# Kernel optimization log

Measured on AMD Instinct MI355X. Metric: run time of the kernel, lower is better.

Reference implementation:

```python
import jax, jax.numpy as jnp
import numpy as np

# ---- config (matches init_kwargs) ----
DIM = 1024
HEADS = 8            # local_heads == heads
QK_HD = 128          # qk_head_dim
V_HD = 128           # v_head_dim
NOPE = 64            # qk_nope_head_dim
ROPE = 64            # qk_rope_head_dim
KV_LORA = 256
N_EXP = 32
N_GROUPS = 8
TOPK = 4             # n_activated_experts
TOPK_GROUPS = 4
INTER = 512
N_SHARED = 1
ROUTE_SCALE = 1.0
EPS = 1e-6


def rmsnorm(x, w):
    xf = x.astype(jnp.float32)
    rms = jnp.sqrt(jnp.mean(xf ** 2, axis=-1, keepdims=True) + EPS)
    return (xf / rms * w).astype(x.dtype)


def setup_inputs() -> dict:
    key = jax.random.key(0)
    ks = jax.random.split(key, 16)
    s = 0.02
    return {
        "x": jax.random.normal(ks[0], (2, 1024, DIM), jnp.float32),
        # attention sub-layer params
        "norm_attn": jnp.ones((DIM,), jnp.float32),
        "wq": jax.random.normal(ks[1], (DIM, HEADS * QK_HD), jnp.float32) * s,
        "wkv_a": jax.random.normal(ks[2], (DIM, KV_LORA + ROPE), jnp.float32) * s,
        "kv_norm_w": jnp.ones((KV_LORA,), jnp.float32),
        "wkv_b": jax.random.normal(ks[3], (KV_LORA, HEADS * (NOPE + V_HD)), jnp.float32) * s,
        "wo": jax.random.normal(ks[4], (HEADS * V_HD, DIM), jnp.float32) * s,
        # MoE sub-layer params
        "norm_moe": jnp.ones((DIM,), jnp.float32),
        "gate_w": jax.random.normal(ks[5], (N_EXP, DIM), jnp.float32) * 0.01,
        "gate_b": jnp.zeros((N_EXP,), jnp.float32),
        "ew1": jax.random.normal(ks[6], (N_EXP, DIM, INTER), jnp.float32) * s,
        "ew2": jax.random.normal(ks[7], (N_EXP, INTER, DIM), jnp.float32) * s,
        "ew3": jax.random.normal(ks[8], (N_EXP, DIM, INTER), jnp.float32) * s,
        "sw1": jax.random.normal(ks[9], (DIM, N_SHARED * INTER), jnp.float32) * s,
        "sw2": jax.random.normal(ks[10], (N_SHARED * INTER, DIM), jnp.float32) * s,
        "sw3": jax.random.normal(ks[11], (DIM, N_SHARED * INTER), jnp.float32) * s,
    }


def _mla(x, wq, wkv_a, kv_norm_w, wkv_b, wo):
    B, S, _ = x.shape
    # q_lora_rank == 0 -> direct q projection; nope/rope split+concat is identity
    q = (x @ wq).reshape(B, S, HEADS, QK_HD)
    kv = x @ wkv_a                                   # [B,S,KV_LORA+ROPE]
    c, k_pe = kv[..., :KV_LORA], kv[..., KV_LORA:]
    kvp = (rmsnorm(c, kv_norm_w) @ wkv_b).reshape(B, S, HEADS, NOPE + V_HD)
    k_nope, v = kvp[..., :NOPE], kvp[..., NOPE:]
    k = jnp.concatenate(
        [k_nope, jnp.broadcast_to(k_pe[:, :, None, :], (B, S, HEADS, ROPE))], axis=-1)
    out = jax.nn.dot_product_attention(q, k, v, scale=QK_HD ** -0.5, is_causal=True)
    return out.reshape(B, S, -1) @ wo


def _gate(xf, gate_w, gate_b):
    T = xf.shape[0]
    scores = jax.nn.sigmoid(xf @ gate_w.T)           # [T,E]
    original = scores
    s = scores + gate_b
    # hierarchical group selection: top-2 score sum per group, keep top groups
    sg = s.reshape(T, N_GROUPS, -1)
    group_score = jnp.sort(sg, axis=-1)[..., -2:].sum(axis=-1)
    group_idx = jnp.argsort(group_score, axis=-1)[..., -TOPK_GROUPS:]
    mask = jnp.ones((T, N_GROUPS), bool).at[jnp.arange(T)[:, None], group_idx].set(False)
    s = jnp.where(mask[..., None], -jnp.inf, sg).reshape(T, -1)
    indices = jnp.argsort(s, axis=-1)[..., -TOPK:]   # [T,K]
    w = jnp.take_along_axis(original, indices, axis=1)
    w = w / (w.sum(axis=-1, keepdims=True) + 1e-20)  # sigmoid normalization
    return w * ROUTE_SCALE, indices


def _moe(xf, gate_w, gate_b, ew1, ew2, ew3, sw1, sw2, sw3):
    # dense all-expert SwiGLU as in the original (nn.vmap over axis_size=E)
    weights, indices = _gate(xf, gate_w, gate_b)
    h = jax.nn.silu(jnp.einsum('td,edh->eth', xf, ew1)) * jnp.einsum('td,edh->eth', xf, ew3)
    all_out = jnp.einsum('eth,ehd->etd', h, ew2)     # [E,T,dim]
    # per-token gather of its top-k experts, weighted combine
    selected = jnp.take_along_axis(all_out.transpose(1, 0, 2), indices[:, :, None], axis=1)  # [T,K,dim]
    y = (selected * weights[..., None]).sum(axis=1)
    z = (jax.nn.silu(xf @ sw1) * (xf @ sw3)) @ sw2   # shared expert MLP
    return y + z


def reference(x, norm_attn, wq, wkv_a, kv_norm_w, wkv_b, wo,
              norm_moe, gate_w, gate_b, ew1, ew2, ew3, sw1, sw2, sw3):
    # MLA layer: x + MLA(RMSNorm(x))
    x = x + _mla(rmsnorm(x, norm_attn), wq, wkv_a, kv_norm_w, wkv_b, wo)
    # MoE layer: x + MoE(RMSNorm(x))
    shape = x.shape
    xf = rmsnorm(x, norm_moe).reshape(-1, DIM)
    y = _moe(xf, gate_w, gate_b, ew1, ew2, ew3, sw1, sw2, sw3)
    return x + y.reshape(shape)
```

## Files before the change

### kernel.cpp

```cpp
#include <hip/hip_runtime.h>
#include <hip/hip_bf16.h>

#define T_TOK 2048
#define DIM 1024
#define HEADS 8
#define QK_HD 128
#define V_HD 128
#define NOPE 64
#define ROPE 64
#define KV_LORA 256
#define N_EXP 32
#define TOPK 4
#define INTER 512
#define S_LEN 1024
#define KVP_W (HEADS * (NOPE + V_HD))

typedef __attribute__((ext_vector_type(8))) _Float16 f16x8;
typedef __attribute__((ext_vector_type(4))) float f32x4;

__device__ inline unsigned short f2h(float f) {
  union { _Float16 h; unsigned short u; } c;
  c.h = (_Float16)f;
  return c.u;
}
__device__ inline float h2f(unsigned short u) {
  union { _Float16 h; unsigned short u; } c;
  c.u = u;
  return (float)c.h;
}

__device__ inline int smask(int row) { return (row & 7) ^ ((row & 3) << 1); }
__device__ inline int swz(int row, int col) {
  return row * 64 + (col ^ (smask(row) << 3));
}

__device__ inline void gl16(const void* g, void* l) {
  __builtin_amdgcn_global_load_lds(
      (const __attribute__((address_space(1))) void*)g,
      (__attribute__((address_space(3))) void*)l, 16, 0, 0);
}

__launch_bounds__(256)
__global__ void tcvt_k(const float* __restrict__ src, unsigned short* __restrict__ dst,
                       int K, int N) {
  int e = blockIdx.z;
  src += (size_t)e * K * N;
  dst += (size_t)e * K * N;
  int n0 = blockIdx.x * 32, k0 = blockIdx.y * 32;
  __shared__ float ts[32][33];
  int tid = threadIdx.x;
  int r = tid >> 3, c4 = (tid & 7) * 4;
  float4 v = *(const float4*)(src + (size_t)(k0 + r) * N + n0 + c4);
  ts[r][c4] = v.x; ts[r][c4 + 1] = v.y; ts[r][c4 + 2] = v.z; ts[r][c4 + 3] = v.w;
  __syncthreads();
  ushort4 o;
  o.x = f2h(ts[c4][r]);
  o.y = f2h(ts[c4 + 1][r]);
  o.z = f2h(ts[c4 + 2][r]);
  o.w = f2h(ts[c4 + 3][r]);
  *(ushort4*)(dst + (size_t)(n0 + r) * K + k0 + c4) = o;
}

__launch_bounds__(64)
__global__ void zero_counters_k(int* __restrict__ counts, int* __restrict__ fill) {
  int i = threadIdx.x;
  if (i < N_EXP) { counts[i] = 0; fill[i] = 0; }
}

__launch_bounds__(256)
__global__ void rmsnorm_k(const float* __restrict__ x, int in_stride, int width,
                          const float* __restrict__ w, unsigned short* __restrict__ out,
                          float* __restrict__ out2, int out_stride) {
  int row = blockIdx.x;
  const float* xr = x + (size_t)row * in_stride;
  float ss = 0.f;
  for (int i = threadIdx.x; i < width; i += 256) { float v = xr[i]; ss += v * v; }
  #pragma unroll
  for (int off = 32; off; off >>= 1) ss += __shfl_down(ss, off, 64);
  __shared__ float red[4];
  if ((threadIdx.x & 63) == 0) red[threadIdx.x >> 6] = ss;
  __syncthreads();
  if (threadIdx.x == 0) {
    float tot = red[0] + red[1] + red[2] + red[3];
    red[0] = rsqrtf(tot / (float)width + 1e-6f);
  }
  __syncthreads();
  float scale = red[0];
  for (int i = threadIdx.x; i < width; i += 256) {
    float v = xr[i] * scale * w[i];
    out[(size_t)row * out_stride + i] = f2h(v);
    if (out2) out2[(size_t)row * out_stride + i] = v;
  }
}

template <int RES, int OUTH>
__launch_bounds__(256)
__global__ void gemm_bt_k(const unsigned short* __restrict__ A,
                          const unsigned short* __restrict__ B,
                          const float* __restrict__ R, void* __restrict__ Cout,
                          int N, int K) {
  const int n0 = blockIdx.x * 64;
  const int m0 = blockIdx.y * 64;
  __shared__ __align__(16) unsigned short As[64 * 64];
  __shared__ __align__(16) unsigned short Bs[64 * 64];
  const int tid = threadIdx.x;
  const int lane = tid & 63, wave = tid >> 6;
  const int quad = lane >> 4, lm = lane & 15;
  const int wm = (wave >> 1) * 32, wn = (wave & 1) * 32;
  f32x4 acc[2][2] = {};
  const int r0 = wave * 16 + (lane >> 3), r1 = r0 + 8;
  const int c0 = ((lane & 7) ^ smask(r0)) * 8;
  const int c1 = ((lane & 7) ^ smask(r1)) * 8;
  const unsigned short* A0 = A + (size_t)(m0 + r0) * K + c0;
  const unsigned short* A1 = A + (size_t)(m0 + r1) * K + c1;
  const unsigned short* B0 = B + (size_t)(n0 + r0) * K + c0;
  const unsigned short* B1 = B + (size_t)(n0 + r1) * K + c1;
  unsigned short* lA0 = &As[(size_t)(wave * 16) * 64];
  unsigned short* lA1 = &As[(size_t)(wave * 16 + 8) * 64];
  unsigned short* lB0 = &Bs[(size_t)(wave * 16) * 64];
  unsigned short* lB1 = &Bs[(size_t)(wave * 16 + 8) * 64];
  for (int k0 = 0; k0 < K; k0 += 64) {
    __syncthreads();
    gl16(A0 + k0, lA0);
    gl16(A1 + k0, lA1);
    gl16(B0 + k0, lB0);
    gl16(B1 + k0, lB1);
    __syncthreads();
    #pragma unroll
    for (int ks = 0; ks < 2; ks++) {
      f16x8 af0 = *(const f16x8*)&As[swz(wm + lm, ks * 32 + quad * 8)];
      f16x8 af1 = *(const f16x8*)&As[swz(wm + 16 + lm, ks * 32 + quad * 8)];
      f16x8 bf0 = *(const f16x8*)&Bs[swz(wn + lm, ks * 32 + quad * 8)];
      f16x8 bf1 = *(const f16x8*)&Bs[swz(wn + 16 + lm, ks * 32 + quad * 8)];
      acc[0][0] = __builtin_amdgcn_mfma_f32_16x16x32_f16(af0, bf0, acc[0][0], 0, 0, 0);
      acc[0][1] = __builtin_amdgcn_mfma_f32_16x16x32_f16(af0, bf1, acc[0][1], 0, 0, 0);
      acc[1][0] = __builtin_amdgcn_mfma_f32_16x16x32_f16(af1, bf0, acc[1][0], 0, 0, 0);
      acc[1][1] = __builtin_amdgcn_mfma_f32_16x16x32_f16(af1, bf1, acc[1][1], 0, 0, 0);
    }
  }
  #pragma unroll
  for (int i = 0; i < 2; i++)
    #pragma unroll
    for (int j = 0; j < 2; j++) {
      int row = m0 + wm + i * 16 + quad * 4;
      int col = n0 + wn + j * 16 + lm;
      #pragma unroll
      for (int r = 0; r < 4; r++) {
        float v = acc[i][j][r];
        if (RES) v += R[(size_t)(row + r) * N + col];
        if (OUTH) ((unsigned short*)Cout)[(size_t)(row + r) * N + col] = f2h(v);
        else ((float*)Cout)[(size_t)(row + r) * N + col] = v;
      }
    }
}

__launch_bounds__(256)
__global__ void moe_up_k(const unsigned short* __restrict__ xfb,
                         const unsigned short* __restrict__ w1t,
                         const unsigned short* __restrict__ w3t,
                         unsigned short* __restrict__ hout,
                         const int* __restrict__ perm, const int* __restrict__ offs,
                         int Mfull) {
  const int e = blockIdx.z;
  int base = 0, count = Mfull;
  if (offs) { base = offs[e]; count = offs[e + 1] - base; }
  const int m0 = blockIdx.y * 64;
  if (m0 >= count) return;
  const int n0 = blockIdx.x * 64;
  const unsigned short* W1 = w1t + (size_t)e * (INTER * DIM);
  const unsigned short* W3 = w3t + (size_t)e * (INTER * DIM);
  __shared__ __align__(16) unsigned short As[64 * 64];
  __shared__ __align__(16) unsigned short B1s[64 * 64];
  __shared__ __align__(16) unsigned short B2s[64 * 64];
  __shared__ int toks[64];
  const int tid = threadIdx.x;
  if (tid < 64) {
    int g = m0 + tid;
    toks[tid] = (g < count) ? (perm ? (perm[base + g] >> 2) : g) : -1;
  }
  __syncthreads();
  const int lane = tid & 63, wave = tid >> 6;
  const int quad = lane >> 4, lm = lane & 15;
  const int wm = (wave >> 1) * 32, wn = (wave & 1) * 32;
  f32x4 acc1[2][2] = {};
  f32x4 acc2[2][2] = {};
  const int r0 = wave * 16 + (lane >> 3), r1 = r0 + 8;
  const int c0 = ((lane & 7) ^ smask(r0)) * 8;
  const int c1 = ((lane & 7) ^ smask(r1)) * 8;
  int tk0 = toks[r0]; if (tk0 < 0) tk0 = 0;
  int tk1 = toks[r1]; if (tk1 < 0) tk1 = 0;
  const unsigned short* A0 = xfb + (size_t)tk0 * DIM + c0;
  const unsigned short* A1 = xfb + (size_t)tk1 * DIM + c1;
  const unsigned short* B10 = W1 + (size_t)(n0 + r0) * DIM + c0;
  const unsigned short* B11 = W1 + (size_t)(n0 + r1) * DIM + c1;
  const unsigned short* B20 = W3 + (size_t)(n0 + r0) * DIM + c0;
  const unsigned short* B21 = W3 + (size_t)(n0 + r1) * DIM + c1;
  unsigned short* lA0 = &As[(size_t)(wave * 16) * 64];
  unsigned short* lA1 = &As[(size_t)(wave * 16 + 8) * 64];
  unsigned short* lB10 = &B1s[(size_t)(wave * 16) * 64];
  unsigned short* lB11 = &B1s[(size_t)(wave * 16 + 8) * 64];
  unsigned short* lB20 = &B2s[(size_t)(wave * 16) * 64];
  unsigned short* lB21 = &B2s[(size_t)(wave * 16 + 8) * 64];
  for (int k0 = 0; k0 < DIM; k0 += 64) {
    __syncthreads();
    gl16(A0 + k0, lA0);
    gl16(A1 + k0, lA1);
    gl16(B10 + k0, lB10);
    gl16(B11 + k0, lB11);
    gl16(B20 + k0, lB20);
    gl16(B21 + k0, lB21);
    __syncthreads();
    #pragma unroll
    for (int ks = 0; ks < 2; ks++) {
      f16x8 af0 = *(const f16x8*)&As[swz(wm + lm, ks * 32 + quad * 8)];
      f16x8 af1 = *(const f16x8*)&As[swz(wm + 16 + lm, ks * 32 + quad * 8)];
      f16x8 b1f0 = *(const f16x8*)&B1s[swz(wn + lm, ks * 32 + quad * 8)];
      f16x8 b1f1 = *(const f16x8*)&B1s[swz(wn + 16 + lm, ks * 32 + quad * 8)];
      f16x8 b2f0 = *(const f16x8*)&B2s[swz(wn + lm, ks * 32 + quad * 8)];
      f16x8 b2f1 = *(const f16x8*)&B2s[swz(wn + 16 + lm, ks * 32 + quad * 8)];
      acc1[0][0] = __builtin_amdgcn_mfma_f32_16x16x32_f16(af0, b1f0, acc1[0][0], 0, 0, 0);
      acc1[0][1] = __builtin_amdgcn_mfma_f32_16x16x32_f16(af0, b1f1, acc1[0][1], 0, 0, 0);
      acc1[1][0] = __builtin_amdgcn_mfma_f32_16x16x32_f16(af1, b1f0, acc1[1][0], 0, 0, 0);
      acc1[1][1] = __builtin_amdgcn_mfma_f32_16x16x32_f16(af1, b1f1, acc1[1][1], 0, 0, 0);
      acc2[0][0] = __builtin_amdgcn_mfma_f32_16x16x32_f16(af0, b2f0, acc2[0][0], 0, 0, 0);
      acc2[0][1] = __builtin_amdgcn_mfma_f32_16x16x32_f16(af0, b2f1, acc2[0][1], 0, 0, 0);
      acc2[1][0] = __builtin_amdgcn_mfma_f32_16x16x32_f16(af1, b2f0, acc2[1][0], 0, 0, 0);
      acc2[1][1] = __builtin_amdgcn_mfma_f32_16x16x32_f16(af1, b2f1, acc2[1][1], 0, 0, 0);
    }
  }
  #pragma unroll
  for (int i = 0; i < 2; i++)
    #pragma unroll
    for (int j = 0; j < 2; j++) {
      int col = n0 + wn + j * 16 + lm;
      #pragma unroll
      for (int r = 0; r < 4; r++) {
        int g = m0 + wm + i * 16 + quad * 4 + r;
        if (g < count) {
          float u = acc1[i][j][r];
          float vv = acc2[i][j][r];
          float h = (u / (1.f + __expf(-u))) * vv;
          hout[(size_t)(base + g) * INTER + col] = f2h(h);
        }
      }
    }
}

__launch_bounds__(256)
__global__ void moe_down_k(const unsigned short* __restrict__ hbuf,
                           const unsigned short* __restrict__ w2t,
                           unsigned short* __restrict__ dout,
                           const int* __restrict__ offs, int Mfull) {
  const int e = blockIdx.z;
  int base = 0, count = Mfull;
  if (offs) { base = offs[e]; count = offs[e + 1] - base; }
  const int m0 = blockIdx.y * 64;
  if (m0 >= count) return;
  const int n0 = blockIdx.x * 64;
  const unsigned short* W2 = w2t + (size_t)e * (DIM * INTER);
  __shared__ __align__(16) unsigned short As[64 * 64];
  __shared__ __align__(16) unsigned short Bs[64 * 64];
  const int tid = threadIdx.x;
  const int lane = tid & 63, wave = tid >> 6;
  const int quad = lane >> 4, lm = lane & 15;
  const int wm = (wave >> 1) * 32, wn = (wave & 1) * 32;
  f32x4 acc[2][2] = {};
  const int r0 = wave * 16 + (lane >> 3), r1 = r0 + 8;
  const int c0 = ((lane & 7) ^ smask(r0)) * 8;
  const int c1 = ((lane & 7) ^ smask(r1)) * 8;
  int g0 = m0 + r0; if (g0 >= count) g0 = 0;
  int g1 = m0 + r1; if (g1 >= count) g1 = 0;
  const unsigned short* A0 = hbuf + (size_t)(base + g0) * INTER + c0;
  const unsigned short* A1 = hbuf + (size_t)(base + g1) * INTER + c1;
  const unsigned short* B0 = W2 + (size_t)(n0 + r0) * INTER + c0;
  const unsigned short* B1 = W2 + (size_t)(n0 + r1) * INTER + c1;
  unsigned short* lA0 = &As[(size_t)(wave * 16) * 64];
  unsigned short* lA1 = &As[(size_t)(wave * 16 + 8) * 64];
  unsigned short* lB0 = &Bs[(size_t)(wave * 16) * 64];
  unsigned short* lB1 = &Bs[(size_t)(wave * 16 + 8) * 64];
  for (int k0 = 0; k0 < INTER; k0 += 64) {
    __syncthreads();
    gl16(A0 + k0, lA0);
    gl16(A1 + k0, lA1);
    gl16(B0 + k0, lB0);
    gl16(B1 + k0, lB1);
    __syncthreads();
    #pragma unroll
    for (int ks = 0; ks < 2; ks++) {
      f16x8 af0 = *(const f16x8*)&As[swz(wm + lm, ks * 32 + quad * 8)];
      f16x8 af1 = *(const f16x8*)&As[swz(wm + 16 + lm, ks * 32 + quad * 8)];
      f16x8 bf0 = *(const f16x8*)&Bs[swz(wn + lm, ks * 32 + quad * 8)];
      f16x8 bf1 = *(const f16x8*)&Bs[swz(wn + 16 + lm, ks * 32 + quad * 8)];
      acc[0][0] = __builtin_amdgcn_mfma_f32_16x16x32_f16(af0, bf0, acc[0][0], 0, 0, 0);
      acc[0][1] = __builtin_amdgcn_mfma_f32_16x16x32_f16(af0, bf1, acc[0][1], 0, 0, 0);
      acc[1][0] = __builtin_amdgcn_mfma_f32_16x16x32_f16(af1, bf0, acc[1][0], 0, 0, 0);
      acc[1][1] = __builtin_amdgcn_mfma_f32_16x16x32_f16(af1, bf1, acc[1][1], 0, 0, 0);
    }
  }
  #pragma unroll
  for (int i = 0; i < 2; i++)
    #pragma unroll
    for (int j = 0; j < 2; j++) {
      int col = n0 + wn + j * 16 + lm;
      #pragma unroll
      for (int r = 0; r < 4; r++) {
        int g = m0 + wm + i * 16 + quad * 4 + r;
        if (g < count)
          dout[(size_t)(base + g) * DIM + col] = f2h(acc[i][j][r]);
      }
    }
}

__launch_bounds__(256)
__global__ void vtrans_k(const unsigned short* __restrict__ kvp,
                         unsigned short* __restrict__ vT) {
  const int z = blockIdx.z, h = z & 7, b = z >> 3;
  const int s0 = blockIdx.x * 32, d0 = blockIdx.y * 32;
  __shared__ unsigned short ts[32][36];
  const int tid = threadIdx.x;
  const int r = tid >> 3, c4 = (tid & 7) * 4;
  ushort4 v = *(const ushort4*)(kvp + (size_t)(b * S_LEN + s0 + r) * KVP_W + h * 192 + 64 + d0 + c4);
  ts[r][c4] = v.x; ts[r][c4 + 1] = v.y; ts[r][c4 + 2] = v.z; ts[r][c4 + 3] = v.w;
  __syncthreads();
  ushort4 o;
  o.x = ts[c4][r]; o.y = ts[c4 + 1][r]; o.z = ts[c4 + 2][r]; o.w = ts[c4 + 3][r];
  *(ushort4*)(vT + ((size_t)z * 128 + d0 + r) * S_LEN + s0 + c4) = o;
}

__launch_bounds__(256)
__global__ void attn_part_k(const unsigned short* __restrict__ q,
                            const unsigned short* __restrict__ kvp,
                            const float* __restrict__ kvb,
                            const unsigned short* __restrict__ vT,
                            float* __restrict__ opart, float* __restrict__ ml) {
  const int qt = blockIdx.x, ch = blockIdx.y, z = blockIdx.z;
  const int kt0 = ch * 4;
  if (kt0 > qt) return;
  const int h = z & 7, b = z >> 3;
  __shared__ __align__(16) _Float16 Ks[64][136];
  __shared__ __align__(16) _Float16 Vt[128][72];
  __shared__ __align__(16) _Float16 Ps[4][16][72];
  const int tid = threadIdx.x;
  const int lane = tid & 63, wave = tid >> 6;
  const int quad = lane >> 4, lm = lane & 15;
  const int qr0 = wave * 16;
  const float scale = 0.08838834764831845f;
  const int tq = b * S_LEN + qt * 64;

  f16x8 qf[4];
  #pragma unroll
  for (int kc = 0; kc < 4; kc++)
    qf[kc] = *(const f16x8*)(q + (size_t)(tq + qr0 + lm) * 1024 + h * 128 + kc * 32 + quad * 8);

  float m_i[4], l_i[4];
  #pragma unroll
  for (int r = 0; r < 4; r++) { m_i[r] = -1e30f; l_i[r] = 0.f; }
  f32x4 o_acc[8] = {};

  const int kt_end = (kt0 + 3 < qt) ? (kt0 + 3) : qt;
  for (int kt = kt0; kt <= kt_end; ++kt) {
    const int tk = b * S_LEN + kt * 64;
    for (int i = tid; i < 64 * 8; i += 256) {
      int key = i & 63, g = i >> 6;
      *(f16x8*)&Ks[key][g * 8] =
          *(const f16x8*)(kvp + (size_t)(tk + key) * KVP_W + h * 192 + g * 8);
    }
    for (int i = tid; i < 64 * 16; i += 256) {
      int key = i & 63, g = i >> 6;
      float4 v = *(const float4*)(kvb + (size_t)(tk + key) * 320 + 256 + g * 4);
      ushort4 u;
      u.x = f2h(v.x); u.y = f2h(v.y); u.z = f2h(v.z); u.w = f2h(v.w);
      *(ushort4*)&Ks[key][64 + g * 4] = u;
    }
    for (int i = tid; i < 128 * 8; i += 256) {
      int d = i >> 3, seg = i & 7;
      *(f16x8*)&Vt[d][seg * 8] =
          *(const f16x8*)(vT + ((size_t)z * 128 + d) * S_LEN + kt * 64 + seg * 8);
    }
    __syncthreads();

    f32x4 sacc[4] = {};
    #pragma unroll
    for (int kc = 0; kc < 4; kc++) {
      #pragma unroll
      for (int jn = 0; jn < 4; jn++) {
        f16x8 bf = *(const f16x8*)&Ks[jn * 16 + lm][kc * 32 + quad * 8];
        sacc[jn] = __builtin_amdgcn_mfma_f32_16x16x32_f16(qf[kc], bf, sacc[jn], 0, 0, 0);
      }
    }
    const bool diag = (kt == qt);
    float p[4][4];
    float rowmax[4], rowsum[4];
    #pragma unroll
    for (int r = 0; r < 4; r++) rowmax[r] = -1e30f;
    #pragma unroll
    for (int jn = 0; jn < 4; jn++)
      #pragma unroll
      for (int r = 0; r < 4; r++) {
        float s = sacc[jn][r] * scale;
        if (diag && (jn * 16 + lm > qr0 + quad * 4 + r)) s = -1e30f;
        p[jn][r] = s;
        rowmax[r] = fmaxf(rowmax[r], s);
      }
    #pragma unroll
    for (int m = 1; m < 16; m <<= 1)
      #pragma unroll
      for (int r = 0; r < 4; r++)
        rowmax[r] = fmaxf(rowmax[r], __shfl_xor(rowmax[r], m, 64));
    float al[4];
    #pragma unroll
    for (int r = 0; r < 4; r++) {
      float mn = fmaxf(m_i[r], rowmax[r]);
      al[r] = __expf(m_i[r] - mn);
      m_i[r] = mn;
      rowsum[r] = 0.f;
    }
    #pragma unroll
    for (int jn = 0; jn < 4; jn++)
      #pragma unroll
      for (int r = 0; r < 4; r++) {
        float pv = __expf(p[jn][r] - m_i[r]);
        p[jn][r] = pv;
        rowsum[r] += pv;
      }
    #pragma unroll
    for (int m = 1; m < 16; m <<= 1)
      #pragma unroll
      for (int r = 0; r < 4; r++)
        rowsum[r] += __shfl_xor(rowsum[r], m, 64);
    #pragma unroll
    for (int r = 0; r < 4; r++) l_i[r] = l_i[r] * al[r] + rowsum[r];
    #pragma unroll
    for (int jn2 = 0; jn2 < 8; jn2++)
      #pragma unroll
      for (int r = 0; r < 4; r++) o_acc[jn2][r] *= al[r];
    #pragma unroll
    for (int jn = 0; jn < 4; jn++)
      #pragma unroll
      for (int r = 0; r < 4; r++)
        Ps[wave][quad * 4 + r][jn * 16 + lm] = (_Float16)p[jn][r];
    #pragma unroll
    for (int kc = 0; kc < 2; kc++) {
      f16x8 af = *(const f16x8*)&Ps[wave][lm][kc * 32 + quad * 8];
      #pragma unroll
      for (int jn2 = 0; jn2 < 8; jn2++) {
        f16x8 bf = *(const f16x8*)&Vt[jn2 * 16 + lm][kc * 32 + quad * 8];
        o_acc[jn2] = __builtin_amdgcn_mfma_f32_16x16x32_f16(af, bf, o_acc[jn2], 0, 0, 0);
      }
    }
    __syncthreads();
  }

  const size_t slot = ((size_t)z * 16 + qt) * 4 + ch;
  float* op = opart + slot * 8192;
  #pragma unroll
  for (int jn2 = 0; jn2 < 8; jn2++) {
    int col = jn2 * 16 + lm;
    #pragma unroll
    for (int r = 0; r < 4; r++) {
      int row = qr0 + quad * 4 + r;
      op[(size_t)row * 128 + col] = o_acc[jn2][r];
    }
  }
  if (lm == 0) {
    #pragma unroll
    for (int r = 0; r < 4; r++) {
      int row = qr0 + quad * 4 + r;
      ml[slot * 128 + row * 2] = m_i[r];
      ml[slot * 128 + row * 2 + 1] = l_i[r];
    }
  }
}

__launch_bounds__(256)
__global__ void attn_comb_k(const float* __restrict__ opart, const float* __restrict__ ml,
                            unsigned short* __restrict__ o) {
  const int qt = blockIdx.x, z = blockIdx.y;
  const int h = z & 7, b = z >> 3;
  const int nch = (qt >> 2) + 1;
  const int tid = threadIdx.x;
  const int colg = tid & 31;
  const int tq = b * S_LEN + qt * 64;
  const size_t slotbase = ((size_t)z * 16 + qt) * 4;
  for (int row = tid >> 5; row < 64; row += 8) {
    float mmax = -1e30f;
    #pragma unroll
    for (int c = 0; c < 4; c++)
      if (c < nch) mmax = fmaxf(mmax, ml[(slotbase + c) * 128 + row * 2]);
    float w[4];
    float lsum = 0.f;
    #pragma unroll
    for (int c = 0; c < 4; c++) {
      if (c < nch) {
        float mc = ml[(slotbase + c) * 128 + row * 2];
        float lc = ml[(slotbase + c) * 128 + row * 2 + 1];
        w[c] = __expf(mc - mmax);
        lsum += lc * w[c];
      } else w[c] = 0.f;
    }
    float inv = 1.f / lsum;
    float ax = 0.f, ay = 0.f, az = 0.f, aw = 0.f;
    #pragma unroll
    for (int c = 0; c < 4; c++) {
      if (c < nch) {
        const float* op = opart + (slotbase + c) * 8192 + (size_t)row * 128 + colg * 4;
        float4 v = *(const float4*)op;
        ax += w[c] * v.x; ay += w[c] * v.y; az += w[c] * v.z; aw += w[c] * v.w;
      }
    }
    ushort4 u;
    u.x = f2h(ax * inv); u.y = f2h(ay * inv);
    u.z = f2h(az * inv); u.w = f2h(aw * inv);
    *(ushort4*)(o + (size_t)(tq + row) * 1024 + h * 128 + colg * 4) = u;
  }
}

__launch_bounds__(256)
__global__ void scores_k(const float* __restrict__ xf, const float* __restrict__ gw,
                         float* __restrict__ sc) {
  __shared__ float xls[32][129];
  __shared__ float gls[32][129];
  const int t0 = blockIdx.x * 32;
  const int tid = threadIdx.x;
  const int lr = tid >> 3, lc = tid & 7;
  const int e = tid & 31, tg = tid >> 5;
  float acc[4] = {};
  for (int k0 = 0; k0 < DIM; k0 += 128) {
    __syncthreads();
    #pragma unroll
    for (int it = 0; it < 4; it++) {
      int col = lc * 4 + it * 32;
      *(float4*)&xls[lr][col] = *(const float4*)(xf + (size_t)(t0 + lr) * DIM + k0 + col);
      *(float4*)&gls[lr][col] = *(const float4*)(gw + (size_t)lr * DIM + k0 + col);
    }
    __syncthreads();
    for (int d = 0; d < 128; d++) {
      float g = gls[e][d];
      #pragma unroll
      for (int j = 0; j < 4; j++)
        acc[j] += xls[tg * 4 + j][d] * g;
    }
  }
  #pragma unroll
  for (int j = 0; j < 4; j++)
    sc[(size_t)(t0 + tg * 4 + j) * N_EXP + e] = acc[j];
}

__launch_bounds__(64)
__global__ void route_k(const float* __restrict__ sc, const float* __restrict__ gb,
                        float* __restrict__ tw, int* __restrict__ tidx,
                        int* __restrict__ counts) {
  int t = blockIdx.x * 64 + threadIdx.x;
  if (t >= T_TOK) return;
  float orig[N_EXP], sb[N_EXP];
  #pragma unroll
  for (int i = 0; i < N_EXP; i++) {
    float s = 1.f / (1.f + __expf(-sc[(size_t)t * N_EXP + i]));
    orig[i] = s;
    sb[i] = s + gb[i];
  }
  float gsc[8];
  #pragma unroll
  for (int g = 0; g < 8; g++) {
    float m1 = -1e30f, m2 = -1e30f;
    #pragma unroll
    for (int j = 0; j < 4; j++) {
      float v = sb[g * 4 + j];
      if (v > m1) { m2 = m1; m1 = v; } else if (v > m2) m2 = v;
    }
    gsc[g] = m1 + m2;
  }
  unsigned gok = 0;
  #pragma unroll
  for (int it = 0; it < 4; it++) {
    int best = 0; float bv = -1e30f;
    #pragma unroll
    for (int g = 0; g < 8; g++)
      if (!((gok >> g) & 1u) && gsc[g] >= bv) { bv = gsc[g]; best = g; }
    gok |= 1u << best;
  }
  unsigned emask = 0;
  #pragma unroll
  for (int g = 0; g < 8; g++)
    if ((gok >> g) & 1u) emask |= 0xFu << (g * 4);
  unsigned taken = 0;
  int idx[TOPK]; float ow[TOPK]; float wsum = 0.f;
  #pragma unroll
  for (int k = 0; k < TOPK; k++) {
    int best = 0; float bv = -1e30f, bo = 0.f;
    #pragma unroll
    for (int i = 0; i < N_EXP; i++)
      if (((emask >> i) & 1u) && !((taken >> i) & 1u) && sb[i] >= bv) {
        bv = sb[i]; best = i; bo = orig[i];
      }
    taken |= 1u << best;
    idx[k] = best; ow[k] = bo; wsum += bo;
  }
  float inv = 1.f / (wsum + 1e-20f);
  #pragma unroll
  for (int k = 0; k < TOPK; k++) {
    tidx[t * TOPK + k] = idx[k];
    tw[t * TOPK + k] = ow[k] * inv;
    atomicAdd(&counts[idx[k]], 1);
  }
}

__global__ void scan_k(const int* __restrict__ counts, int* __restrict__ offs) {
  if (threadIdx.x == 0 && blockIdx.x == 0) {
    int acc = 0;
    for (int e = 0; e < N_EXP; e++) { offs[e] = acc; acc += counts[e]; }
    offs[N_EXP] = acc;
  }
}

__launch_bounds__(256)
__global__ void scatter_k(const int* __restrict__ tidx, const int* __restrict__ offs,
                          int* __restrict__ fill, int* __restrict__ perm,
                          int* __restrict__ posOf) {
  int t = blockIdx.x * 256 + threadIdx.x;
  if (t >= T_TOK) return;
  for (int j = 0; j < TOPK; j++) {
    int e = tidx[t * TOPK + j];
    int pos = atomicAdd(&fill[e], 1);
    int p = offs[e] + pos;
    perm[p] = t * TOPK + j;
    posOf[t * TOPK + j] = p;
  }
}

__launch_bounds__(256)
__global__ void final_gather_k(const float* __restrict__ x1,
                               const unsigned short* __restrict__ dbuf,
                               const unsigned short* __restrict__ sdbuf,
                               const int* __restrict__ posOf,
                               const float* __restrict__ tw,
                               float* __restrict__ out) {
  int t = blockIdx.x;
  int c0 = threadIdx.x * 4;
  int p0 = posOf[t * 4 + 0], p1 = posOf[t * 4 + 1];
  int p2 = posOf[t * 4 + 2], p3 = posOf[t * 4 + 3];
  float w0 = tw[t * 4 + 0], w1 = tw[t * 4 + 1];
  float w2 = tw[t * 4 + 2], w3 = tw[t * 4 + 3];
  size_t tb = (size_t)t * DIM;
  #pragma unroll
  for (int i = 0; i < 4; i++) {
    int c = c0 + i;
    float v = x1[tb + c] + h2f(sdbuf[tb + c])
            + w0 * h2f(dbuf[(size_t)p0 * DIM + c])
            + w1 * h2f(dbuf[(size_t)p1 * DIM + c])
            + w2 * h2f(dbuf[(size_t)p2 * DIM + c])
            + w3 * h2f(dbuf[(size_t)p3 * DIM + c]);
    out[tb + c] = v;
  }
}

extern "C" void kernel_launch(void* const* d_in, const int* in_sizes, int n_in,
                              void* d_out, int out_size, void* d_ws, size_t ws_size,
                              hipStream_t stream) {
  const float* x        = (const float*)d_in[0];
  const float* norm_attn= (const float*)d_in[1];
  const float* wq       = (const float*)d_in[2];
  const float* wkv_a    = (const float*)d_in[3];
  const float* kv_norm_w= (const float*)d_in[4];
  const float* wkv_b    = (const float*)d_in[5];
  const float* wo       = (const float*)d_in[6];
  const float* norm_moe = (const float*)d_in[7];
  const float* gate_w   = (const float*)d_in[8];
  const float* gate_b   = (const float*)d_in[9];
  const float* ew1      = (const float*)d_in[10];
  const float* ew2      = (const float*)d_in[11];
  const float* ew3      = (const float*)d_in[12];
  const float* sw1      = (const float*)d_in[13];
  const float* sw2      = (const float*)d_in[14];
  const float* sw3      = (const float*)d_in[15];
  float* out = (float*)d_out;

  char* wp = (char*)d_ws;
  auto alloc = [&](size_t bytes) -> char* {
    char* r = wp;
    wp += (bytes + 255) & ~(size_t)255;
    return r;
  };
  typedef unsigned short us;
  us* wqT   = (us*)alloc(1048576 * 2);
  us* wkvaT = (us*)alloc(327680 * 2);
  us* wkvbT = (us*)alloc(393216 * 2);
  us* woT   = (us*)alloc(1048576 * 2);
  us* ew1T  = (us*)alloc((size_t)16777216 * 2);
  us* ew3T  = (us*)alloc((size_t)16777216 * 2);
  us* ew2T  = (us*)alloc((size_t)16777216 * 2);
  us* sw1T  = (us*)alloc(524288 * 2);
  us* sw3T  = (us*)alloc(524288 * 2);
  us* sw2T  = (us*)alloc(524288 * 2);
  us* xb    = (us*)alloc(2097152 * 2);
  us* cn    = (us*)alloc(524288 * 2);
  us* atn   = (us*)alloc(2097152 * 2);
  us* dbuf  = (us*)alloc((size_t)8388608 * 2);
  us* qb    = (us*)alloc(2097152 * 4);
  float* kvb  = (float*)alloc(655360 * 4);
  us* kvp   = (us*)alloc(3145728 * 4);
  float* x1   = (float*)alloc(2097152 * 4);
  float* xf32 = (float*)alloc(2097152 * 4);
  float* scb  = (float*)alloc(65536 * 4);
  float* twb  = (float*)alloc(8192 * 4);
  int* tidx   = (int*)alloc(8192 * 4);
  int* perm   = (int*)alloc(8192 * 4);
  int* posOf  = (int*)alloc(8192 * 4);
  int* counts = (int*)alloc(64 * 4);
  int* offs   = (int*)alloc(64 * 4);
  int* fill   = (int*)alloc(64 * 4);
  us* vT     = (us*)alloc((size_t)2 * 8 * 128 * 1024 * 2);
  float* mlb = (float*)alloc((size_t)1024 * 128 * 4);
  us* sdbuf = qb;
  us* hbuf  = kvp;
  us* hs    = hbuf + (size_t)8192 * 512;
  float* opart = (float*)ew1T;

  tcvt_k<<<dim3(32, 32, 1), 256, 0, stream>>>(wq, wqT, 1024, 1024);
  tcvt_k<<<dim3(10, 32, 1), 256, 0, stream>>>(wkv_a, wkvaT, 1024, 320);
  tcvt_k<<<dim3(48, 8, 1), 256, 0, stream>>>(wkv_b, wkvbT, 256, 1536);
  tcvt_k<<<dim3(32, 32, 1), 256, 0, stream>>>(wo, woT, 1024, 1024);

  rmsnorm_k<<<T_TOK, 256, 0, stream>>>(x, DIM, DIM, norm_attn, xb, nullptr, DIM);
  gemm_bt_k<0, 1><<<dim3(16, 32), 256, 0, stream>>>(xb, wqT, nullptr, qb, 1024, 1024);
  gemm_bt_k<0, 0><<<dim3(5, 32), 256, 0, stream>>>(xb, wkvaT, nullptr, kvb, 320, 1024);
  rmsnorm_k<<<T_TOK, 256, 0, stream>>>(kvb, 320, KV_LORA, kv_norm_w, cn, nullptr, KV_LORA);
  gemm_bt_k<0, 1><<<dim3(24, 32), 256, 0, stream>>>(cn, wkvbT, nullptr, kvp, 1536, 256);
  vtrans_k<<<dim3(32, 4, 16), 256, 0, stream>>>(kvp, vT);
  attn_part_k<<<dim3(16, 4, 16), 256, 0, stream>>>(qb, kvp, kvb, vT, opart, mlb);
  attn_comb_k<<<dim3(16, 16), 256, 0, stream>>>(opart, mlb, atn);
  gemm_bt_k<1, 0><<<dim3(16, 32), 256, 0, stream>>>(atn, woT, x, x1, 1024, 1024);

  tcvt_k<<<dim3(16, 32, 32), 256, 0, stream>>>(ew1, ew1T, 1024, 512);
  tcvt_k<<<dim3(16, 32, 32), 256, 0, stream>>>(ew3, ew3T, 1024, 512);
  tcvt_k<<<dim3(32, 16, 32), 256, 0, stream>>>(ew2, ew2T, 512, 1024);
  tcvt_k<<<dim3(16, 32, 1), 256, 0, stream>>>(sw1, sw1T, 1024, 512);
  tcvt_k<<<dim3(16, 32, 1), 256, 0, stream>>>(sw3, sw3T, 1024, 512);
  tcvt_k<<<dim3(32, 16, 1), 256, 0, stream>>>(sw2, sw2T, 512, 1024);

  rmsnorm_k<<<T_TOK, 256, 0, stream>>>(x1, DIM, DIM, norm_moe, xb, xf32, DIM);
  zero_counters_k<<<1, 64, 0, stream>>>(counts, fill);
  scores_k<<<T_TOK / 32, 256, 0, stream>>>(xf32, gate_w, scb);
  route_k<<<T_TOK / 64, 64, 0, stream>>>(scb, gate_b, twb, tidx, counts);
  scan_k<<<1, 1, 0, stream>>>(counts, offs);
  scatter_k<<<(T_TOK + 255) / 256, 256, 0, stream>>>(tidx, offs, fill, perm, posOf);
  moe_up_k<<<dim3(8, 32, 32), 256, 0, stream>>>(xb, ew1T, ew3T, hbuf, perm, offs, 0);
  moe_down_k<<<dim3(16, 32, 32), 256, 0, stream>>>(hbuf, ew2T, dbuf, offs, 0);
  moe_up_k<<<dim3(8, 32, 1), 256, 0, stream>>>(xb, sw1T, sw3T, hs, nullptr, nullptr, T_TOK);
  moe_down_k<<<dim3(16, 32, 1), 256, 0, stream>>>(hs, sw2T, sdbuf, nullptr, T_TOK);

  final_gather_k<<<T_TOK, 256, 0, stream>>>(x1, dbuf, sdbuf, posOf, twb, out);
}
```

Baseline: 550.9 us.

## Register-prefetch gemm tiles and merge shared expert into routed MoE launches

The generic GEMM now loads the next K-tile into registers while the current tile is computed, replacing direct global-to-LDS loads with a register double-buffer that hides global latency. Separately, the shared-expert up and down projections are folded into the routed-expert kernels as an extra z-slice, cutting two launches and letting shared work fill idle CUs alongside the routed experts. The cost is more registers in the GEMM and a per-block branch on expert index.

```diff
diff --git a/kernel.cpp b/kernel.cpp
--- a/kernel.cpp
+++ b/kernel.cpp
@@ -108,24 +108,27 @@
   const int quad = lane >> 4, lm = lane & 15;
   const int wm = (wave >> 1) * 32, wn = (wave & 1) * 32;
   f32x4 acc[2][2] = {};
-  const int r0 = wave * 16 + (lane >> 3), r1 = r0 + 8;
-  const int c0 = ((lane & 7) ^ smask(r0)) * 8;
-  const int c1 = ((lane & 7) ^ smask(r1)) * 8;
-  const unsigned short* A0 = A + (size_t)(m0 + r0) * K + c0;
-  const unsigned short* A1 = A + (size_t)(m0 + r1) * K + c1;
-  const unsigned short* B0 = B + (size_t)(n0 + r0) * K + c0;
-  const unsigned short* B1 = B + (size_t)(n0 + r1) * K + c1;
-  unsigned short* lA0 = &As[(size_t)(wave * 16) * 64];
-  unsigned short* lA1 = &As[(size_t)(wave * 16 + 8) * 64];
-  unsigned short* lB0 = &Bs[(size_t)(wave * 16) * 64];
-  unsigned short* lB1 = &Bs[(size_t)(wave * 16 + 8) * 64];
+  const int sr = tid >> 2, sc = tid & 3;
+  const unsigned short* Ap = A + (size_t)(m0 + sr) * K;
+  const unsigned short* Bp = B + (size_t)(n0 + sr) * K;
+  f16x8 a0 = *(const f16x8*)(Ap + sc * 8);
+  f16x8 a1 = *(const f16x8*)(Ap + sc * 8 + 32);
+  f16x8 b0 = *(const f16x8*)(Bp + sc * 8);
+  f16x8 b1 = *(const f16x8*)(Bp + sc * 8 + 32);
   for (int k0 = 0; k0 < K; k0 += 64) {
     __syncthreads();
-    gl16(A0 + k0, lA0);
-    gl16(A1 + k0, lA1);
-    gl16(B0 + k0, lB0);
-    gl16(B1 + k0, lB1);
-    __syncthreads();
+    *(f16x8*)&As[swz(sr, sc * 8)] = a0;
+    *(f16x8*)&As[swz(sr, sc * 8 + 32)] = a1;
+    *(f16x8*)&Bs[swz(sr, sc * 8)] = b0;
+    *(f16x8*)&Bs[swz(sr, sc * 8 + 32)] = b1;
+    __syncthreads();
+    const int kn = k0 + 64;
+    if (kn < K) {
+      a0 = *(const f16x8*)(Ap + kn + sc * 8);
+      a1 = *(const f16x8*)(Ap + kn + sc * 8 + 32);
+      b0 = *(const f16x8*)(Bp + kn + sc * 8);
+      b1 = *(const f16x8*)(Bp + kn + sc * 8 + 32);
+    }
     #pragma unroll
     for (int ks = 0; ks < 2; ks++) {
       f16x8 af0 = *(const f16x8*)&As[swz(wm + lm, ks * 32 + quad * 8)];
@@ -158,17 +161,21 @@
 __global__ void moe_up_k(const unsigned short* __restrict__ xfb,
                          const unsigned short* __restrict__ w1t,
                          const unsigned short* __restrict__ w3t,
+                         const unsigned short* __restrict__ sw1t,
+                         const unsigned short* __restrict__ sw3t,
                          unsigned short* __restrict__ hout,
-                         const int* __restrict__ perm, const int* __restrict__ offs,
-                         int Mfull) {
+                         unsigned short* __restrict__ hs,
+                         const int* __restrict__ perm, const int* __restrict__ offs) {
   const int e = blockIdx.z;
-  int base = 0, count = Mfull;
-  if (offs) { base = offs[e]; count = offs[e + 1] - base; }
+  const bool se = (e == N_EXP);
+  const int base = se ? 0 : offs[e];
+  const int count = se ? T_TOK : (offs[e + 1] - base);
   const int m0 = blockIdx.y * 64;
   if (m0 >= count) return;
   const int n0 = blockIdx.x * 64;
-  const unsigned short* W1 = w1t + (size_t)e * (INTER * DIM);
-  const unsigned short* W3 = w3t + (size_t)e * (INTER * DIM);
+  const unsigned short* W1 = se ? sw1t : (w1t + (size_t)e * (INTER * DIM));
+  const unsigned short* W3 = se ? sw3t : (w3t + (size_t)e * (INTER * DIM));
+  unsigned short* H = se ? hs : hout;
   __shared__ __align__(16) unsigned short As[64 * 64];
   __shared__ __align__(16) unsigned short B1s[64 * 64];
   __shared__ __align__(16) unsigned short B2s[64 * 64];
@@ -176,7 +183,7 @@
   const int tid = threadIdx.x;
   if (tid < 64) {
     int g = m0 + tid;
-    toks[tid] = (g < count) ? (perm ? (perm[base + g] >> 2) : g) : -1;
+    toks[tid] = (g < count) ? (se ? g : (perm[base + g] >> 2)) : -1;
   }
   __syncthreads();
   const int lane = tid & 63, wave = tid >> 6;
@@ -240,7 +247,7 @@
           float u = acc1[i][j][r];
           float vv = acc2[i][j][r];
           float h = (u / (1.f + __expf(-u))) * vv;
-          hout[(size_t)(base + g) * INTER + col] = f2h(h);
+          H[(size_t)(base + g) * INTER + col] = f2h(h);
         }
       }
     }
@@ -248,16 +255,22 @@
 
 __launch_bounds__(256)
 __global__ void moe_down_k(const unsigned short* __restrict__ hbuf,
+                           const unsigned short* __restrict__ hs,
                            const unsigned short* __restrict__ w2t,
-                           unsigned short* __restrict__ dout,
-                           const int* __restrict__ offs, int Mfull) {
+                           const unsigned short* __restrict__ sw2t,
+                           unsigned short* __restrict__ dbuf,
+                           unsigned short* __restrict__ sdbuf,
+                           const int* __restrict__ offs) {
   const int e = blockIdx.z;
-  int base = 0, count = Mfull;
-  if (offs) { base = offs[e]; count = offs[e + 1] - base; }
+  const bool se = (e == N_EXP);
+  const int base = se ? 0 : offs[e];
+  const int count = se ? T_TOK : (offs[e + 1] - base);
   const int m0 = blockIdx.y * 64;
   if (m0 >= count) return;
   const int n0 = blockIdx.x * 64;
-  const unsigned short* W2 = w2t + (size_t)e * (DIM * INTER);
+  const unsigned short* W2 = se ? sw2t : (w2t + (size_t)e * (DIM * INTER));
+  const unsigned short* Hsrc = se ? hs : hbuf;
+  unsigned short* Dout = se ? sdbuf : dbuf;
   __shared__ __align__(16) unsigned short As[64 * 64];
   __shared__ __align__(16) unsigned short Bs[64 * 64];
   const int tid = threadIdx.x;
@@ -270,8 +283,8 @@
   const int c1 = ((lane & 7) ^ smask(r1)) * 8;
   int g0 = m0 + r0; if (g0 >= count) g0 = 0;
   int g1 = m0 + r1; if (g1 >= count) g1 = 0;
-  const unsigned short* A0 = hbuf + (size_t)(base + g0) * INTER + c0;
-  const unsigned short* A1 = hbuf + (size_t)(base + g1) * INTER + c1;
+  const unsigned short* A0 = Hsrc + (size_t)(base + g0) * INTER + c0;
+  const unsigned short* A1 = Hsrc + (size_t)(base + g1) * INTER + c1;
   const unsigned short* B0 = W2 + (size_t)(n0 + r0) * INTER + c0;
   const unsigned short* B1 = W2 + (size_t)(n0 + r1) * INTER + c1;
   unsigned short* lA0 = &As[(size_t)(wave * 16) * 64];
@@ -306,7 +319,7 @@
       for (int r = 0; r < 4; r++) {
         int g = m0 + wm + i * 16 + quad * 4 + r;
         if (g < count)
-          dout[(size_t)(base + g) * DIM + col] = f2h(acc[i][j][r]);
+          Dout[(size_t)(base + g) * DIM + col] = f2h(acc[i][j][r]);
       }
     }
 }
@@ -744,10 +757,10 @@
   route_k<<<T_TOK / 64, 64, 0, stream>>>(scb, gate_b, twb, tidx, counts);
   scan_k<<<1, 1, 0, stream>>>(counts, offs);
   scatter_k<<<(T_TOK + 255) / 256, 256, 0, stream>>>(tidx, offs, fill, perm, posOf);
-  moe_up_k<<<dim3(8, 32, 32), 256, 0, stream>>>(xb, ew1T, ew3T, hbuf, perm, offs, 0);
-  moe_down_k<<<dim3(16, 32, 32), 256, 0, stream>>>(hbuf, ew2T, dbuf, offs, 0);
-  moe_up_k<<<dim3(8, 32, 1), 256, 0, stream>>>(xb, sw1T, sw3T, hs, nullptr, nullptr, T_TOK);
-  moe_down_k<<<dim3(16, 32, 1), 256, 0, stream>>>(hs, sw2T, sdbuf, nullptr, T_TOK);
+  moe_up_k<<<dim3(8, 32, N_EXP + 1), 256, 0, stream>>>(xb, ew1T, ew3T, sw1T, sw3T,
+                                                       hbuf, hs, perm, offs);
+  moe_down_k<<<dim3(16, 32, N_EXP + 1), 256, 0, stream>>>(hbuf, hs, ew2T, sw2T,
+                                                          dbuf, sdbuf, offs);
 
   final_gather_k<<<T_TOK, 256, 0, stream>>>(x1, dbuf, sdbuf, posOf, twb, out);
 }
```

Result: faster. 531.1 us (-3.6%).
